# Performance work log

Measured on AMD Instinct MI355X. Metric: run time of the kernel, lower is better.

The kernel has to match this reference:

```python
import jax, jax.numpy as jnp
import numpy as np

N = 50000   # nodes per graph
E = 800000  # edges per graph
FIN = 128   # node_features
H = 4       # heads
C = 32      # out channels per head (hidden_dim // heads)
HID = H * C # 128
FE = 16     # edge_features
B = 8       # graphs in batch
NEG_SLOPE = 0.2


def setup_inputs() -> dict:
    key = jax.random.key(0)
    ks = jax.random.split(key, 30)
    f32 = jnp.float32
    inp = {
        'x_a': jax.random.normal(ks[0], (N, FIN), f32),
        'edge_index_a': jax.random.randint(ks[1], (2, E), 0, N),
        'edge_attr_a': jax.random.normal(ks[2], (E, FE), f32),
        'batch_a': jnp.sort(jax.random.randint(ks[3], (N,), 0, B)),
        'x_b': jax.random.normal(ks[4], (N, FIN), f32),
        'edge_index_b': jax.random.randint(ks[5], (2, E), 0, N),
        'edge_attr_b': jax.random.normal(ks[6], (E, FE), f32),
        'batch_b': jnp.sort(jax.random.randint(ks[7], (N,), 0, B)),
    }
    def p(i, shape, s=0.05):
        return jax.random.normal(ks[i], shape, f32) * s
    # GAT layer 1 (in FIN -> H*C)
    inp['W1l'] = p(8, (FIN, HID)); inp['b1l'] = jnp.zeros((HID,), f32)
    inp['W1r'] = p(9, (FIN, HID)); inp['b1r'] = jnp.zeros((HID,), f32)
    inp['W1e'] = p(10, (FE, HID))
    inp['att1'] = p(11, (H, C))
    inp['bias1'] = jnp.zeros((HID,), f32)
    # GAT layer 2 (in HID -> H*C)
    inp['W2l'] = p(12, (HID, HID)); inp['b2l'] = jnp.zeros((HID,), f32)
    inp['W2r'] = p(13, (HID, HID)); inp['b2r'] = jnp.zeros((HID,), f32)
    inp['W2e'] = p(14, (FE, HID))
    inp['att2'] = p(15, (H, C))
    inp['bias2'] = jnp.zeros((HID,), f32)
    # fc head: Linear(4*HID, HID) -> ReLU -> Linear(HID, 1)
    inp['Wf1'] = p(16, (4 * HID, HID)); inp['bf1'] = jnp.zeros((HID,), f32)
    inp['Wf2'] = p(17, (HID, 1)); inp['bf2'] = jnp.zeros((1,), f32)
    return inp


def gatv2(x, edge_index, edge_attr, Wl, bl, Wr, br, We, att, bias):
    """GATv2Conv (concat=True), eval mode (no dropout)."""
    src, dst = edge_index[0], edge_index[1]
    n = x.shape[0]
    xl = (x @ Wl + bl).reshape(n, H, C)  # source transform
    xr = (x @ Wr + br).reshape(n, H, C)  # target transform
    # per-edge pre-activation: x_j + x_i + edge_emb  -> [E, H, C]
    m = xl[src] + xr[dst] + (edge_attr @ We).reshape(-1, H, C)
    logits = jnp.einsum('ehc,hc->eh', jax.nn.leaky_relu(m, NEG_SLOPE), att)  # [E, H]
    # scatter-softmax over incoming edges of each destination node
    lmax = jax.ops.segment_max(logits, dst, num_segments=n)
    lmax = jnp.where(jnp.isfinite(lmax), lmax, 0.0)
    ex = jnp.exp(logits - lmax[dst])
    denom = jax.ops.segment_sum(ex, dst, num_segments=n)
    alpha = ex / (denom[dst] + 1e-16)  # [E, H]
    out = jax.ops.segment_sum(alpha[:, :, None] * xl[src], dst, num_segments=n)  # [N, H, C]
    return out.reshape(n, HID) + bias


def encode(x, edge_index, edge_attr, batch,
           W1l, b1l, W1r, b1r, W1e, att1, bias1,
           W2l, b2l, W2r, b2r, W2e, att2, bias2):
    h = jax.nn.elu(gatv2(x, edge_index, edge_attr, W1l, b1l, W1r, b1r, W1e, att1, bias1))
    h = jax.nn.elu(gatv2(h, edge_index, edge_attr, W2l, b2l, W2r, b2r, W2e, att2, bias2))
    cnt = jnp.clip(jax.ops.segment_sum(jnp.ones((h.shape[0],), h.dtype), batch, num_segments=B), 1.0)
    h_mean = jax.ops.segment_sum(h, batch, num_segments=B) / cnt[:, None]
    h_max = jax.ops.segment_max(h, batch, num_segments=B)
    h_max = jnp.where(jnp.isfinite(h_max), h_max, 0.0)
    return jnp.concatenate([h_mean, h_max], axis=-1)  # [B, 2*HID]


def reference(x_a, edge_index_a, edge_attr_a, batch_a,
              x_b, edge_index_b, edge_attr_b, batch_b,
              W1l, b1l, W1r, b1r, W1e, att1, bias1,
              W2l, b2l, W2r, b2r, W2e, att2, bias2,
              Wf1, bf1, Wf2, bf2):
    emb_a = encode(x_a, edge_index_a, edge_attr_a, batch_a,
                   W1l, b1l, W1r, b1r, W1e, att1, bias1,
                   W2l, b2l, W2r, b2r, W2e, att2, bias2)
    emb_b = encode(x_b, edge_index_b, edge_attr_b, batch_b,
                   W1l, b1l, W1r, b1r, W1e, att1, bias1,
                   W2l, b2l, W2r, b2r, W2e, att2, bias2)
    combined = jnp.concatenate([emb_a, emb_b], axis=-1)  # [B, 4*HID]
    hidden = jax.nn.relu(combined @ Wf1 + bf1)
    dominance = jax.nn.sigmoid(hidden @ Wf2 + bf2).squeeze(-1)  # [B]
    return dominance
```

## Files before the change

### kernel.cpp

```cpp
#include <hip/hip_runtime.h>
#include <hip/hip_fp16.h>

#define NN 50000
#define NE 800000
#define HIDD 128
#define FEAT_E 16
#define NGRAPH 8
#define CAP 64

typedef __attribute__((ext_vector_type(2))) _Float16 half2_t;
typedef __attribute__((ext_vector_type(8))) _Float16 half8_t;
typedef __attribute__((ext_vector_type(4))) float floatx4;


__device__ __forceinline__ unsigned int fenc(float f) {
  unsigned int u = __float_as_uint(f);
  return (u & 0x80000000u) ? ~u : (u | 0x80000000u);
}
__device__ __forceinline__ float fdec(unsigned int u) {
  if (u == 0u) return 0.0f;
  float f = (u & 0x80000000u) ? __uint_as_float(u & 0x7fffffffu)
                              : __uint_as_float(~u);
  return __builtin_isfinite(f) ? f : 0.0f;
}

__device__ __forceinline__ half8_t splat8(_Float16 v) {
  return (half8_t){v, v, v, v, v, v, v, v};
}
__device__ __forceinline__ half8_t hmax8(half8_t a, half8_t b) {
#if __has_builtin(__builtin_elementwise_max)
  return __builtin_elementwise_max(a, b);
#else
  half8_t r;
#pragma unroll
  for (int i = 0; i < 8; ++i) r[i] = a[i] > b[i] ? a[i] : b[i];
  return r;
#endif
}
__device__ __forceinline__ float dot_att(half8_t lk, half2_t t01, half2_t t23,
                                         half2_t t45, half2_t t67) {
#if __has_builtin(__builtin_amdgcn_fdot2)
  float p = __builtin_amdgcn_fdot2((half2_t){lk[0], lk[1]}, t01, 0.f, false);
  p = __builtin_amdgcn_fdot2((half2_t){lk[2], lk[3]}, t23, p, false);
  p = __builtin_amdgcn_fdot2((half2_t){lk[4], lk[5]}, t45, p, false);
  p = __builtin_amdgcn_fdot2((half2_t){lk[6], lk[7]}, t67, p, false);
  return p;
#else
  float p = 0.f;
  p += (float)lk[0] * (float)t01[0] + (float)lk[1] * (float)t01[1];
  p += (float)lk[2] * (float)t23[0] + (float)lk[3] * (float)t23[1];
  p += (float)lk[4] * (float)t45[0] + (float)lk[5] * (float)t45[1];
  p += (float)lk[6] * (float)t67[0] + (float)lk[7] * (float)t67[1];
  return p;
#endif
}

__global__ void prep_wt_k(const float* __restrict__ Wl, const float* __restrict__ Wr,
                          _Float16* __restrict__ wtg) {
  const int r = blockIdx.x & 127;
  const int which = blockIdx.x >> 7;
  const int k = threadIdx.x;
  const float* W = which ? Wr : Wl;
  const int oc_src = (r & 15) * 8 + (r >> 4);
  const int col = k ^ ((r & 7) << 3);
  wtg[(which * 128 + r) * 128 + col] = (_Float16)W[k * 128 + oc_src];
}

__device__ __forceinline__ half8_t load_a8(const _Float16* p) {
  return *(const half8_t*)p;
}
__device__ __forceinline__ half8_t load_a8(const float* p) {
  const float4 f0 = *(const float4*)p;
  const float4 f1 = *(const float4*)(p + 4);
  return (half8_t){(_Float16)f0.x, (_Float16)f0.y, (_Float16)f0.z, (_Float16)f0.w,
                   (_Float16)f1.x, (_Float16)f1.y, (_Float16)f1.z, (_Float16)f1.w};
}

template <typename TIN>
__global__ __launch_bounds__(256) void node_linear_mfma_k(
    const TIN* __restrict__ x, const _Float16* __restrict__ wtg,
    const float* __restrict__ bl, const float* __restrict__ br,
    _Float16* __restrict__ xl16, _Float16* __restrict__ xr16) {
  __shared__ _Float16 wt[128 * 128];
  const int tid = threadIdx.x;
  const int which = blockIdx.y;
  const _Float16* wsrc = wtg + which * (128 * 128);
  const float* bias128 = which ? br : bl;
  _Float16* out = which ? xr16 : xl16;
  {
    const half8_t* src = (const half8_t*)wsrc;
    half8_t* dstl = (half8_t*)wt;
#pragma unroll
    for (int it = 0; it < 8; ++it)
      dstl[it * 256 + tid] = src[it * 256 + tid];
  }
  __syncthreads();

  const int wv = tid >> 6, lane = tid & 63;
  const int arow = lane & 15, kq = lane >> 4;
  const int nbase = blockIdx.x * 64 + wv * 16;
  int nload = nbase + arow;
  if (nload >= NN) nload = NN - 1;
  floatx4 acc[8];
#pragma unroll
  for (int t = 0; t < 8; ++t) acc[t] = (floatx4){0.f, 0.f, 0.f, 0.f};
#pragma unroll
  for (int kb = 0; kb < 4; ++kb) {
    const half8_t a = load_a8(x + (size_t)nload * 128 + kb * 32 + kq * 8);
    const int colbase = (kb * 32 + kq * 8) ^ ((arow & 7) << 3);
#pragma unroll
    for (int t = 0; t < 8; ++t) {
      const half8_t b = *(const half8_t*)&wt[(t * 16 + arow) * 128 + colbase];
      acc[t] = __builtin_amdgcn_mfma_f32_16x16x32_f16(a, b, acc[t], 0, 0, 0);
    }
  }
  const float4 bv0 = *(const float4*)&bias128[arow * 8];
  const float4 bv1 = *(const float4*)&bias128[arow * 8 + 4];
  const float bv[8] = {bv0.x, bv0.y, bv0.z, bv0.w, bv1.x, bv1.y, bv1.z, bv1.w};
#pragma unroll
  for (int i = 0; i < 4; ++i) {
    const int n = nbase + kq * 4 + i;
    if (n < NN) {
      half8_t v;
#pragma unroll
      for (int t = 0; t < 8; ++t) v[t] = (_Float16)(acc[t][i] + bv[t]);
      *(half8_t*)(out + (size_t)n * 128 + arow * 8) = v;
    }
  }
}

__global__ void build_k(const int* __restrict__ src, const int* __restrict__ dst,
                        const float* __restrict__ eattr,
                        int* __restrict__ cnt, int2* __restrict__ bpair,
                        _Float16* __restrict__ eatt16) {
  const int e = blockIdx.x * blockDim.x + threadIdx.x;
  if (e >= NE) return;
  const float4* ea = (const float4*)(eattr + (size_t)e * FEAT_E);
  const float4 a0 = ea[0], a1 = ea[1], a2 = ea[2], a3 = ea[3];
  half8_t h0 = {(_Float16)a0.x, (_Float16)a0.y, (_Float16)a0.z, (_Float16)a0.w,
                (_Float16)a1.x, (_Float16)a1.y, (_Float16)a1.z, (_Float16)a1.w};
  half8_t h1 = {(_Float16)a2.x, (_Float16)a2.y, (_Float16)a2.z, (_Float16)a2.w,
                (_Float16)a3.x, (_Float16)a3.y, (_Float16)a3.z, (_Float16)a3.w};
  half8_t* eo = (half8_t*)(eatt16 + (size_t)e * FEAT_E);
  eo[0] = h0; eo[1] = h1;
  const int d = dst[e];
  const int pos = atomicAdd(&cnt[d], 1);
  if (pos < CAP) bpair[(size_t)d * CAP + pos] = make_int2(src[e], e);
}

__global__ __launch_bounds__(256) void node_gat_fused_k(
    const _Float16* __restrict__ xl16, const _Float16* __restrict__ xr16,
    const _Float16* __restrict__ eatt16,
    const int2* __restrict__ bpair, const int* __restrict__ cnt,
    const float* __restrict__ We, const float* __restrict__ att,
    const float* __restrict__ bias, _Float16* __restrict__ hout) {
  __shared__ half8_t WeS[FEAT_E][16];
  const int tid = threadIdx.x;
  {
    const int f = tid >> 4, q = tid & 15;
    const float4 w0 = ((const float4*)We)[f * 32 + q * 2];
    const float4 w1 = ((const float4*)We)[f * 32 + q * 2 + 1];
    WeS[f][q] = (half8_t){(_Float16)w0.x, (_Float16)w0.y, (_Float16)w0.z, (_Float16)w0.w,
                          (_Float16)w1.x, (_Float16)w1.y, (_Float16)w1.z, (_Float16)w1.w};
  }
  __syncthreads();

  const int wave = tid >> 6, lane = tid & 63;
  const int slot = lane >> 4, l16 = lane & 15;
  const int d = blockIdx.x * 4 + wave;

  const float4 af0 = ((const float4*)att)[l16 * 2];
  const float4 af1 = ((const float4*)att)[l16 * 2 + 1];
  const half2_t at01 = {(_Float16)af0.x, (_Float16)af0.y};
  const half2_t at23 = {(_Float16)af0.z, (_Float16)af0.w};
  const half2_t at45 = {(_Float16)af1.x, (_Float16)af1.y};
  const half2_t at67 = {(_Float16)af1.z, (_Float16)af1.w};

  const half8_t xrh = *(const half8_t*)(xr16 + (size_t)d * HIDD + l16 * 8);

  int deg = cnt[d];
  deg = deg < CAP ? deg : CAP;
  const int2* bp = bpair + (size_t)d * CAP;

  float acc0 = 0.f, acc1 = 0.f, acc2 = 0.f, acc3 = 0.f;
  float acc4 = 0.f, acc5 = 0.f, acc6 = 0.f, acc7 = 0.f;
  float den = 0.f;

#define FINISH_EDGE(XL, EM)                                              \
  {                                                                      \
    half8_t m_ = ((XL) + xrh) + (EM);                                    \
    half8_t lk_ = hmax8(m_, m_ * splat8((_Float16)0.2f));                \
    float p_ = dot_att(lk_, at01, at23, at45, at67);                     \
    p_ += __shfl_xor(p_, 1);                                             \
    p_ += __shfl_xor(p_, 2);                                             \
    const float w_ = __expf(p_);                                         \
    den += w_;                                                           \
    acc0 = fmaf(w_, (float)(XL)[0], acc0);                               \
    acc1 = fmaf(w_, (float)(XL)[1], acc1);                               \
    acc2 = fmaf(w_, (float)(XL)[2], acc2);                               \
    acc3 = fmaf(w_, (float)(XL)[3], acc3);                               \
    acc4 = fmaf(w_, (float)(XL)[4], acc4);                               \
    acc5 = fmaf(w_, (float)(XL)[5], acc5);                               \
    acc6 = fmaf(w_, (float)(XL)[6], acc6);                               \
    acc7 = fmaf(w_, (float)(XL)[7], acc7);                               \
  }

  int j = slot;
  for (; j + 4 < deg; j += 8) {
    const int2 p0 = bp[j];
    const int2 p1 = bp[j + 4];
    const half8_t x0 = *(const half8_t*)(xl16 + (unsigned)p0.x * 128u + l16 * 8);
    const half8_t x1 = *(const half8_t*)(xl16 + (unsigned)p1.x * 128u + l16 * 8);
    const half8_t a0 = *(const half8_t*)(eatt16 + (unsigned)p0.y * 16u);
    const half8_t b0 = *(const half8_t*)(eatt16 + (unsigned)p0.y * 16u + 8u);
    const half8_t a1 = *(const half8_t*)(eatt16 + (unsigned)p1.y * 16u);
    const half8_t b1 = *(const half8_t*)(eatt16 + (unsigned)p1.y * 16u + 8u);
    half8_t em0 = {}, em1 = {};
#pragma unroll
    for (int f = 0; f < 8; ++f) {
      const half8_t wf = WeS[f][l16];
      em0 += splat8(a0[f]) * wf;
      em1 += splat8(a1[f]) * wf;
    }
#pragma unroll
    for (int f = 0; f < 8; ++f) {
      const half8_t wf = WeS[8 + f][l16];
      em0 += splat8(b0[f]) * wf;
      em1 += splat8(b1[f]) * wf;
    }
    FINISH_EDGE(x0, em0)
    FINISH_EDGE(x1, em1)
  }
  if (j < deg) {
    const int2 p0 = bp[j];
    const half8_t x0 = *(const half8_t*)(xl16 + (unsigned)p0.x * 128u + l16 * 8);
    const half8_t a0 = *(const half8_t*)(eatt16 + (unsigned)p0.y * 16u);
    const half8_t b0 = *(const half8_t*)(eatt16 + (unsigned)p0.y * 16u + 8u);
    half8_t em0 = {};
#pragma unroll
    for (int f = 0; f < 8; ++f) em0 += splat8(a0[f]) * WeS[f][l16];
#pragma unroll
    for (int f = 0; f < 8; ++f) em0 += splat8(b0[f]) * WeS[8 + f][l16];
    FINISH_EDGE(x0, em0)
  }
#undef FINISH_EDGE

#define RED(A) A += __shfl_xor(A, 16); A += __shfl_xor(A, 32);
  RED(acc0) RED(acc1) RED(acc2) RED(acc3)
  RED(acc4) RED(acc5) RED(acc6) RED(acc7)
  RED(den)
#undef RED
  if (slot == 0) {
    const float inv = 1.f / (den + 1e-16f);
    const float4 b0 = ((const float4*)bias)[l16 * 2];
    const float4 b1 = ((const float4*)bias)[l16 * 2 + 1];
    float o0 = fmaf(acc0, inv, b0.x), o1 = fmaf(acc1, inv, b0.y);
    float o2 = fmaf(acc2, inv, b0.z), o3 = fmaf(acc3, inv, b0.w);
    float o4 = fmaf(acc4, inv, b1.x), o5 = fmaf(acc5, inv, b1.y);
    float o6 = fmaf(acc6, inv, b1.z), o7 = fmaf(acc7, inv, b1.w);
    o0 = o0 > 0.f ? o0 : expm1f(o0);  o1 = o1 > 0.f ? o1 : expm1f(o1);
    o2 = o2 > 0.f ? o2 : expm1f(o2);  o3 = o3 > 0.f ? o3 : expm1f(o3);
    o4 = o4 > 0.f ? o4 : expm1f(o4);  o5 = o5 > 0.f ? o5 : expm1f(o5);
    o6 = o6 > 0.f ? o6 : expm1f(o6);  o7 = o7 > 0.f ? o7 : expm1f(o7);
    half8_t ho = {(_Float16)o0, (_Float16)o1, (_Float16)o2, (_Float16)o3,
                  (_Float16)o4, (_Float16)o5, (_Float16)o6, (_Float16)o7};
    *(half8_t*)(hout + (size_t)d * HIDD + l16 * 8) = ho;
  }
}

__global__ void pool_k(const _Float16* __restrict__ h, const int* __restrict__ batch,
                       float* __restrict__ gsum, unsigned int* __restrict__ gmax,
                       float* __restrict__ gcnt) {
  __shared__ float ssum[NGRAPH][HIDD];
  __shared__ float smax[NGRAPH][HIDD];
  __shared__ float scnt[NGRAPH];
  const int t = threadIdx.x;
#pragma unroll
  for (int g = 0; g < NGRAPH; ++g) {
    ssum[g][t] = 0.f;
    smax[g][t] = -3.0e38f;
  }
  if (t < NGRAPH) scnt[t] = 0.f;
  __syncthreads();
  const int n0 = blockIdx.x * 64;
  const int nEnd = (n0 + 64 < NN) ? (n0 + 64) : NN;
  unsigned int seen = 0;
  for (int n = n0; n < nEnd; ++n) {
    const int g = batch[n];
    seen |= 1u << g;
    const float v = (float)h[(size_t)n * HIDD + t];
    ssum[g][t] += v;
    smax[g][t] = fmaxf(smax[g][t], v);
    if (t == 0) scnt[g] += 1.f;
  }
  __syncthreads();
  for (int g = 0; g < NGRAPH; ++g) {
    if (seen & (1u << g)) {
      atomicAdd(&gsum[g * HIDD + t], ssum[g][t]);
      atomicMax(&gmax[g * HIDD + t], fenc(smax[g][t]));
      if (t == 0) atomicAdd(&gcnt[g], scnt[g]);
    }
  }
}

__global__ void head_k(const float* __restrict__ suma, const unsigned int* __restrict__ maxa,
                       const float* __restrict__ cnta,
                       const float* __restrict__ sumb, const unsigned int* __restrict__ maxb,
                       const float* __restrict__ cntb,
                       const float* __restrict__ Wf1, const float* __restrict__ bf1,
                       const float* __restrict__ Wf2, const float* __restrict__ bf2,
                       float* __restrict__ out) {
  __shared__ float c[4 * HIDD];
  __shared__ float red[HIDD];
  const int g = blockIdx.x, t = threadIdx.x;
  const float ca = fmaxf(cnta[g], 1.f), cb = fmaxf(cntb[g], 1.f);
  c[t]            = suma[g * HIDD + t] / ca;
  c[HIDD + t]     = fdec(maxa[g * HIDD + t]);
  c[2 * HIDD + t] = sumb[g * HIDD + t] / cb;
  c[3 * HIDD + t] = fdec(maxb[g * HIDD + t]);
  __syncthreads();
  float acc = bf1[t];
  for (int i = 0; i < 4 * HIDD; ++i)
    acc = fmaf(c[i], Wf1[(size_t)i * HIDD + t], acc);
  acc = fmaxf(acc, 0.f);
  red[t] = acc * Wf2[t];
  __syncthreads();
  for (int s2 = 64; s2 > 0; s2 >>= 1) {
    if (t < s2) red[t] += red[t + s2];
    __syncthreads();
  }
  if (t == 0) out[g] = 1.f / (1.f + expf(-(red[0] + bf2[0])));
}

extern "C" void kernel_launch(void* const* d_in, const int* in_sizes, int n_in,
                              void* d_out, int out_size, void* d_ws, size_t ws_size,
                              hipStream_t stream) {
  (void)in_sizes; (void)n_in; (void)out_size; (void)ws_size;
  const float* xA    = (const float*)d_in[0];
  const int*   eiA   = (const int*)  d_in[1];
  const float* eaA   = (const float*)d_in[2];
  const int*   batA  = (const int*)  d_in[3];
  const float* xB    = (const float*)d_in[4];
  const int*   eiB   = (const int*)  d_in[5];
  const float* eaB   = (const float*)d_in[6];
  const int*   batB  = (const int*)  d_in[7];
  const float* W1l   = (const float*)d_in[8];
  const float* b1l   = (const float*)d_in[9];
  const float* W1r   = (const float*)d_in[10];
  const float* b1r   = (const float*)d_in[11];
  const float* W1e   = (const float*)d_in[12];
  const float* att1  = (const float*)d_in[13];
  const float* bias1 = (const float*)d_in[14];
  const float* W2l   = (const float*)d_in[15];
  const float* b2l   = (const float*)d_in[16];
  const float* W2r   = (const float*)d_in[17];
  const float* b2r   = (const float*)d_in[18];
  const float* W2e   = (const float*)d_in[19];
  const float* att2  = (const float*)d_in[20];
  const float* bias2 = (const float*)d_in[21];
  const float* Wf1   = (const float*)d_in[22];
  const float* bf1   = (const float*)d_in[23];
  const float* Wf2   = (const float*)d_in[24];
  const float* bf2   = (const float*)d_in[25];

  char* ws = (char*)d_ws;
  size_t off = 0;
  auto alloc = [&](size_t bytes) -> void* {
    void* p = ws + off;
    off += (bytes + 255) & ~(size_t)255;
    return p;
  };
  _Float16* h16    = (_Float16*)alloc((size_t)NN * HIDD * 2);
  _Float16* xl16   = (_Float16*)alloc((size_t)NN * HIDD * 2);
  _Float16* xr16   = (_Float16*)alloc((size_t)NN * HIDD * 2);
  int2*     bpair  = (int2*)    alloc((size_t)NN * CAP * 8);
  _Float16* eatt16 = (_Float16*)alloc((size_t)NE * FEAT_E * 2);
  int*      cnt    = (int*)     alloc((size_t)NN * 4);
  _Float16* wtg1   = (_Float16*)alloc(2 * 128 * 128 * 2);
  _Float16* wtg2   = (_Float16*)alloc(2 * 128 * 128 * 2);
  const size_t poolStart = off;
  float*        psumA = (float*)alloc(NGRAPH * HIDD * 4);
  unsigned int* pmaxA = (unsigned int*)alloc(NGRAPH * HIDD * 4);
  float*        pcntA = (float*)alloc(NGRAPH * 4);
  float*        psumB = (float*)alloc(NGRAPH * HIDD * 4);
  unsigned int* pmaxB = (unsigned int*)alloc(NGRAPH * HIDD * 4);
  float*        pcntB = (float*)alloc(NGRAPH * 4);
  const size_t poolBytes = off - poolStart;

  const float* xs[2]   = {xA, xB};
  const int*   eis[2]  = {eiA, eiB};
  const float* eas[2]  = {eaA, eaB};
  const int*   bats[2] = {batA, batB};
  float*        psums[2] = {psumA, psumB};
  unsigned int* pmaxs[2] = {pmaxA, pmaxB};
  float*        pcnts[2] = {pcntA, pcntB};

  hipMemsetAsync(psumA, 0, poolBytes, stream);
  prep_wt_k<<<256, 128, 0, stream>>>(W1l, W1r, wtg1);
  prep_wt_k<<<256, 128, 0, stream>>>(W2l, W2r, wtg2);

  for (int g = 0; g < 2; ++g) {
    const int* src = eis[g];
    const int* dst = eis[g] + NE;
    hipMemsetAsync(cnt, 0, (size_t)NN * 4, stream);
    build_k<<<NE / 256, 256, 0, stream>>>(src, dst, eas[g], cnt, bpair, eatt16);
    node_linear_mfma_k<float><<<dim3((NN + 63) / 64, 2), 256, 0, stream>>>(
        xs[g], wtg1, b1l, b1r, xl16, xr16);
    node_gat_fused_k<<<NN / 4, 256, 0, stream>>>(xl16, xr16, eatt16, bpair, cnt,
                                                 W1e, att1, bias1, h16);
    node_linear_mfma_k<_Float16><<<dim3((NN + 63) / 64, 2), 256, 0, stream>>>(
        h16, wtg2, b2l, b2r, xl16, xr16);
    node_gat_fused_k<<<NN / 4, 256, 0, stream>>>(xl16, xr16, eatt16, bpair, cnt,
                                                 W2e, att2, bias2, h16);
    pool_k<<<(NN + 63) / 64, 128, 0, stream>>>(h16, bats[g], psums[g], pmaxs[g], pcnts[g]);
  }
  head_k<<<NGRAPH, 128, 0, stream>>>(psumA, pmaxA, pcntA, psumB, pmaxB, pcntB,
                                     Wf1, bf1, Wf2, bf2, (float*)d_out);
}
```

Baseline: 852.3 us.

## Preload edge pairs per lane and software-pipeline gather loads in GAT aggregation

Each lane loads one (src, edge id) pair for the node up front, and iterations broadcast the indices with shuffles instead of reloading them from global memory. The edge loop is software-pipelined so the gathers of xl and edge attributes for the next group of edges are issued before the current group is computed. Invalid lanes are masked by zeroing their attention weight rather than by branching. The aim is to hide gather latency and remove dependent index loads, at the cost of more live registers and some wasted work on padded edges.

```diff
diff --git a/kernel.cpp b/kernel.cpp
--- a/kernel.cpp
+++ b/kernel.cpp
@@ -180,20 +180,22 @@
 
   int deg = cnt[d];
   deg = deg < CAP ? deg : CAP;
-  const int2* bp = bpair + (size_t)d * CAP;
+
+  int2 myp = make_int2(0, 0);
+  if (lane < deg) myp = bpair[(size_t)d * CAP + lane];
 
   float acc0 = 0.f, acc1 = 0.f, acc2 = 0.f, acc3 = 0.f;
   float acc4 = 0.f, acc5 = 0.f, acc6 = 0.f, acc7 = 0.f;
   float den = 0.f;
 
-#define FINISH_EDGE(XL, EM)                                              \
+#define FINISH_EDGE(XL, EM, VALID)                                       \
   {                                                                      \
     half8_t m_ = ((XL) + xrh) + (EM);                                    \
     half8_t lk_ = hmax8(m_, m_ * splat8((_Float16)0.2f));                \
     float p_ = dot_att(lk_, at01, at23, at45, at67);                     \
     p_ += __shfl_xor(p_, 1);                                             \
     p_ += __shfl_xor(p_, 2);                                             \
-    const float w_ = __expf(p_);                                         \
+    const float w_ = (VALID) ? __expf(p_) : 0.f;                         \
     den += w_;                                                           \
     acc0 = fmaf(w_, (float)(XL)[0], acc0);                               \
     acc1 = fmaf(w_, (float)(XL)[1], acc1);                               \
@@ -205,44 +207,61 @@
     acc7 = fmaf(w_, (float)(XL)[7], acc7);                               \
   }
 
-  int j = slot;
-  for (; j + 4 < deg; j += 8) {
-    const int2 p0 = bp[j];
-    const int2 p1 = bp[j + 4];
-    const half8_t x0 = *(const half8_t*)(xl16 + (unsigned)p0.x * 128u + l16 * 8);
-    const half8_t x1 = *(const half8_t*)(xl16 + (unsigned)p1.x * 128u + l16 * 8);
-    const half8_t a0 = *(const half8_t*)(eatt16 + (unsigned)p0.y * 16u);
-    const half8_t b0 = *(const half8_t*)(eatt16 + (unsigned)p0.y * 16u + 8u);
-    const half8_t a1 = *(const half8_t*)(eatt16 + (unsigned)p1.y * 16u);
-    const half8_t b1 = *(const half8_t*)(eatt16 + (unsigned)p1.y * 16u + 8u);
-    half8_t em0 = {}, em1 = {};
-#pragma unroll
-    for (int f = 0; f < 8; ++f) {
-      const half8_t wf = WeS[f][l16];
-      em0 += splat8(a0[f]) * wf;
-      em1 += splat8(a1[f]) * wf;
+#define LOAD_PAIR_AT(E0, E1, X0, X1, A0, B0, A1, B1)                     \
+  {                                                                      \
+    const int s0_ = __shfl(myp.x, (E0)), i0_ = __shfl(myp.y, (E0));      \
+    const int s1_ = __shfl(myp.x, (E1)), i1_ = __shfl(myp.y, (E1));      \
+    X0 = *(const half8_t*)(xl16 + (unsigned)s0_ * 128u + l16 * 8);       \
+    X1 = *(const half8_t*)(xl16 + (unsigned)s1_ * 128u + l16 * 8);       \
+    A0 = *(const half8_t*)(eatt16 + (unsigned)i0_ * 16u);                \
+    B0 = *(const half8_t*)(eatt16 + (unsigned)i0_ * 16u + 8u);           \
+    A1 = *(const half8_t*)(eatt16 + (unsigned)i1_ * 16u);                \
+    B1 = *(const half8_t*)(eatt16 + (unsigned)i1_ * 16u + 8u);           \
+  }
+
+#define COMPUTE_PAIR()                                                   \
+  {                                                                      \
+    half8_t em0 = {}, em1 = {};                                          \
+    _Pragma("unroll") for (int f = 0; f < 8; ++f) {                      \
+      const half8_t wf = WeS[f][l16];                                    \
+      em0 += splat8(a0[f]) * wf;                                         \
+      em1 += splat8(a1[f]) * wf;                                         \
+    }                                                                    \
+    _Pragma("unroll") for (int f = 0; f < 8; ++f) {                      \
+      const half8_t wf = WeS[8 + f][l16];                                \
+      em0 += splat8(b0[f]) * wf;                                         \
+      em1 += splat8(b1[f]) * wf;                                         \
+    }                                                                    \
+    FINISH_EDGE(x0, em0, e0 < deg)                                       \
+    FINISH_EDGE(x1, em1, e1 < deg)                                       \
+  }
+
+  const int T = (deg + 7) >> 3;
+  if (T > 0) {
+    int e0 = slot, e1 = slot + 4;
+    half8_t x0, x1, a0, b0, a1, b1;
+    LOAD_PAIR_AT(e0, e1, x0, x1, a0, b0, a1, b1)
+    for (int k = 0; k + 1 < T; ++k) {
+      half8_t nx0, nx1, na0, nb0, na1, nb1;
+      LOAD_PAIR_AT(e0 + 8, e1 + 8, nx0, nx1, na0, nb0, na1, nb1)
+      COMPUTE_PAIR()
+      e0 += 8; e1 += 8;
+      x0 = nx0; x1 = nx1; a0 = na0; b0 = nb0; a1 = na1; b1 = nb1;
     }
-#pragma unroll
-    for (int f = 0; f < 8; ++f) {
-      const half8_t wf = WeS[8 + f][l16];
-      em0 += splat8(b0[f]) * wf;
-      em1 += splat8(b1[f]) * wf;
+    const bool pairLast = (((T - 1) << 3) + 4) < deg;
+    if (pairLast) {
+      COMPUTE_PAIR()
+    } else {
+      half8_t em0 = {};
+#pragma unroll
+      for (int f = 0; f < 8; ++f) em0 += splat8(a0[f]) * WeS[f][l16];
+#pragma unroll
+      for (int f = 0; f < 8; ++f) em0 += splat8(b0[f]) * WeS[8 + f][l16];
+      FINISH_EDGE(x0, em0, e0 < deg)
     }
-    FINISH_EDGE(x0, em0)
-    FINISH_EDGE(x1, em1)
-  }
-  if (j < deg) {
-    const int2 p0 = bp[j];
-    const half8_t x0 = *(const half8_t*)(xl16 + (unsigned)p0.x * 128u + l16 * 8);
-    const half8_t a0 = *(const half8_t*)(eatt16 + (unsigned)p0.y * 16u);
-    const half8_t b0 = *(const half8_t*)(eatt16 + (unsigned)p0.y * 16u + 8u);
-    half8_t em0 = {};
-#pragma unroll
-    for (int f = 0; f < 8; ++f) em0 += splat8(a0[f]) * WeS[f][l16];
-#pragma unroll
-    for (int f = 0; f < 8; ++f) em0 += splat8(b0[f]) * WeS[8 + f][l16];
-    FINISH_EDGE(x0, em0)
-  }
+  }
+#undef COMPUTE_PAIR
+#undef LOAD_PAIR_AT
 #undef FINISH_EDGE
 
 #define RED(A) A += __shfl_xor(A, 16); A += __shfl_xor(A, 32);
```

Measured after the change: 797.4 us. -6.4%, faster.

## Software-pipeline GAT edge gathers with wave-wide index preload and triple buffering

Applied to the files above, without the earlier changes.

Each lane loads one (src, edge id) pair from the bucketed edge list up front, and the pairs are distributed with shuffles. A three-stage register ring prefetches neighbor features and edge attributes two iterations ahead of the compute. This is meant to hide gather latency in the per-destination aggregation loop. In exchange it raises register pressure, which may cut occupancy, and adds masked work for padded edges.

```diff
diff --git a/kernel.cpp b/kernel.cpp
--- a/kernel.cpp
+++ b/kernel.cpp
@@ -176,24 +176,25 @@
   const half2_t at45 = {(_Float16)af1.x, (_Float16)af1.y};
   const half2_t at67 = {(_Float16)af1.z, (_Float16)af1.w};
 
+  int deg = cnt[d];
+  int2 myp = bpair[(size_t)d * CAP + lane];
   const half8_t xrh = *(const half8_t*)(xr16 + (size_t)d * HIDD + l16 * 8);
-
-  int deg = cnt[d];
   deg = deg < CAP ? deg : CAP;
-  const int2* bp = bpair + (size_t)d * CAP;
+  myp.x = ((unsigned)myp.x < NN) ? myp.x : 0;
+  myp.y = ((unsigned)myp.y < NE) ? myp.y : 0;
 
   float acc0 = 0.f, acc1 = 0.f, acc2 = 0.f, acc3 = 0.f;
   float acc4 = 0.f, acc5 = 0.f, acc6 = 0.f, acc7 = 0.f;
   float den = 0.f;
 
-#define FINISH_EDGE(XL, EM)                                              \
+#define FINISH_EDGE(XL, EM, VALID)                                       \
   {                                                                      \
     half8_t m_ = ((XL) + xrh) + (EM);                                    \
     half8_t lk_ = hmax8(m_, m_ * splat8((_Float16)0.2f));                \
     float p_ = dot_att(lk_, at01, at23, at45, at67);                     \
     p_ += __shfl_xor(p_, 1);                                             \
     p_ += __shfl_xor(p_, 2);                                             \
-    const float w_ = __expf(p_);                                         \
+    const float w_ = (VALID) ? __expf(p_) : 0.f;                         \
     den += w_;                                                           \
     acc0 = fmaf(w_, (float)(XL)[0], acc0);                               \
     acc1 = fmaf(w_, (float)(XL)[1], acc1);                               \
@@ -205,44 +206,71 @@
     acc7 = fmaf(w_, (float)(XL)[7], acc7);                               \
   }
 
-  int j = slot;
-  for (; j + 4 < deg; j += 8) {
-    const int2 p0 = bp[j];
-    const int2 p1 = bp[j + 4];
-    const half8_t x0 = *(const half8_t*)(xl16 + (unsigned)p0.x * 128u + l16 * 8);
-    const half8_t x1 = *(const half8_t*)(xl16 + (unsigned)p1.x * 128u + l16 * 8);
-    const half8_t a0 = *(const half8_t*)(eatt16 + (unsigned)p0.y * 16u);
-    const half8_t b0 = *(const half8_t*)(eatt16 + (unsigned)p0.y * 16u + 8u);
-    const half8_t a1 = *(const half8_t*)(eatt16 + (unsigned)p1.y * 16u);
-    const half8_t b1 = *(const half8_t*)(eatt16 + (unsigned)p1.y * 16u + 8u);
-    half8_t em0 = {}, em1 = {};
-#pragma unroll
-    for (int f = 0; f < 8; ++f) {
-      const half8_t wf = WeS[f][l16];
-      em0 += splat8(a0[f]) * wf;
-      em1 += splat8(a1[f]) * wf;
+  half8_t PX0[3], PX1[3], PA0[3], PB0[3], PA1[3], PB1[3];
+
+#define LOADSET(S, K)                                                    \
+  {                                                                      \
+    const int eA_ = slot + 8 * (K), eB_ = slot + 4 + 8 * (K);            \
+    const int sA_ = __shfl(myp.x, eA_), iA_ = __shfl(myp.y, eA_);        \
+    const int sB_ = __shfl(myp.x, eB_), iB_ = __shfl(myp.y, eB_);        \
+    PX0[S] = *(const half8_t*)(xl16 + (unsigned)sA_ * 128u + l16 * 8);   \
+    PX1[S] = *(const half8_t*)(xl16 + (unsigned)sB_ * 128u + l16 * 8);   \
+    PA0[S] = *(const half8_t*)(eatt16 + (unsigned)iA_ * 16u);            \
+    PB0[S] = *(const half8_t*)(eatt16 + (unsigned)iA_ * 16u + 8u);       \
+    PA1[S] = *(const half8_t*)(eatt16 + (unsigned)iB_ * 16u);            \
+    PB1[S] = *(const half8_t*)(eatt16 + (unsigned)iB_ * 16u + 8u);       \
+  }
+
+#define COMPUTE_K(S, K)                                                  \
+  {                                                                      \
+    const int e0_ = slot + 8 * (K);                                      \
+    if (8 * (K) + 4 < deg) {                \
+      const int e1_ = e0_ + 4;                                           \
+      half8_t em0 = {}, em1 = {};                                        \
+      _Pragma("unroll") for (int f = 0; f < 8; ++f) {                    \
+        const half8_t wf = WeS[f][l16];                                  \
+        em0 += splat8(PA0[S][f]) * wf;                                   \
+        em1 += splat8(PA1[S][f]) * wf;                                   \
+      }                                                                  \
+      _Pragma("unroll") for (int f = 0; f < 8; ++f) {                    \
+        const half8_t wf = WeS[8 + f][l16];                              \
+        em0 += splat8(PB0[S][f]) * wf;                                   \
+        em1 += splat8(PB1[S][f]) * wf;                                   \
+      }                                                                  \
+      FINISH_EDGE(PX0[S], em0, e0_ < deg)                                \
+      FINISH_EDGE(PX1[S], em1, e1_ < deg)                                \
+    } else {                         \
+      half8_t em0 = {};                                                  \
+      _Pragma("unroll") for (int f = 0; f < 8; ++f)                      \
+        em0 += splat8(PA0[S][f]) * WeS[f][l16];                          \
+      _Pragma("unroll") for (int f = 0; f < 8; ++f)                      \
+        em0 += splat8(PB0[S][f]) * WeS[8 + f][l16];                      \
+      FINISH_EDGE(PX0[S], em0, e0_ < deg)                                \
+    }                                                                    \
+  }
+
+  const int T = (deg + 7) >> 3;
+  if (T > 0) LOADSET(0, 0)
+  if (T > 1) LOADSET(1, 1)
+#pragma unroll
+  for (int k = 0; k < 8; ++k) {
+    if (k < T) {
+      if (k + 2 < T) {
+        switch ((k + 2) % 3) {
+          case 0: LOADSET(0, k + 2) break;
+          case 1: LOADSET(1, k + 2) break;
+          default: LOADSET(2, k + 2) break;
+        }
+      }
+      switch (k % 3) {
+        case 0: COMPUTE_K(0, k) break;
+        case 1: COMPUTE_K(1, k) break;
+        default: COMPUTE_K(2, k) break;
+      }
     }
-#pragma unroll
-    for (int f = 0; f < 8; ++f) {
-      const half8_t wf = WeS[8 + f][l16];
-      em0 += splat8(b0[f]) * wf;
-      em1 += splat8(b1[f]) * wf;
-    }
-    FINISH_EDGE(x0, em0)
-    FINISH_EDGE(x1, em1)
-  }
-  if (j < deg) {
-    const int2 p0 = bp[j];
-    const half8_t x0 = *(const half8_t*)(xl16 + (unsigned)p0.x * 128u + l16 * 8);
-    const half8_t a0 = *(const half8_t*)(eatt16 + (unsigned)p0.y * 16u);
-    const half8_t b0 = *(const half8_t*)(eatt16 + (unsigned)p0.y * 16u + 8u);
-    half8_t em0 = {};
-#pragma unroll
-    for (int f = 0; f < 8; ++f) em0 += splat8(a0[f]) * WeS[f][l16];
-#pragma unroll
-    for (int f = 0; f < 8; ++f) em0 += splat8(b0[f]) * WeS[8 + f][l16];
-    FINISH_EDGE(x0, em0)
-  }
+  }
+#undef COMPUTE_K
+#undef LOADSET
 #undef FINISH_EDGE
 
 #define RED(A) A += __shfl_xor(A, 16); A += __shfl_xor(A, 32);
@@ -251,9 +279,9 @@
   RED(den)
 #undef RED
   if (slot == 0) {
-    const float inv = 1.f / (den + 1e-16f);
     const float4 b0 = ((const float4*)bias)[l16 * 2];
     const float4 b1 = ((const float4*)bias)[l16 * 2 + 1];
+    const float inv = 1.f / (den + 1e-16f);
     float o0 = fmaf(acc0, inv, b0.x), o1 = fmaf(acc1, inv, b0.y);
     float o2 = fmaf(acc2, inv, b0.z), o3 = fmaf(acc3, inv, b0.w);
     float o4 = fmaf(acc4, inv, b1.x), o5 = fmaf(acc5, inv, b1.y);
```

New measurement: 806.1 us. 5.4% less time.
